# Kernel optimization log

Hardware: AMD Instinct MI355X
Metric: run time of the kernel (lower is better)

## Reference

```python
import jax, jax.numpy as jnp
import numpy as np

DIM = 192
STATE = 64
B = 8
H = 64
W = 64
EPS_LN = 1e-5
EPS_BN = 1e-5


def _layernorm(x, g, b):
    m = jnp.mean(x, axis=-1, keepdims=True)
    v = jnp.mean((x - m) ** 2, axis=-1, keepdims=True)
    return (x - m) / jnp.sqrt(v + EPS_LN) * g + b


def _linear(x, w, b=None):
    # torch Linear convention: w is [out, in]
    y = jnp.einsum('...i,oi->...o', x, w)
    return y if b is None else y + b


def _parallel_scan(A, Bd, xp):
    # A, Bd, xp: [B, L, S]; h_t = A_t*h_{t-1} + Bd_t*xp_t via log-space cumsum
    A_safe = jnp.clip(A, 0.001, 0.999)
    log_A = jnp.log(A_safe + 1e-10)
    log_cum_A = jnp.cumsum(log_A, axis=1)
    log_cum_A_max = jnp.max(log_cum_A, axis=1, keepdims=True)
    cum_A = jnp.exp(log_cum_A - log_cum_A_max)
    BX = Bd * xp
    # prepend zeros, drop last: normalizer uses cumprod up to t-1
    log_pad = jnp.pad(log_cum_A - log_cum_A_max, ((0, 0), (1, 0), (0, 0)))[:, :-1]
    BX_norm = BX * jnp.exp(-log_pad)
    return jnp.cumsum(BX_norm, axis=1) * cum_A


def _ssm(x, ln_g, ln_b, xp_w, xp_b, dt_w, dt_b, A_log, B_w, C_w, Dp, out_w, out_b):
    xn = _layernorm(x, ln_g, ln_b)
    delta = jax.nn.softplus(_linear(xn, dt_w, dt_b)) * 0.01 + 0.0001  # [B,L,S]
    B_t = _linear(xn, B_w)
    C_t = _linear(xn, C_w)
    A = -jnp.exp(A_log)  # [S]
    x_proj = _linear(xn, xp_w, xp_b)
    deltaA = jnp.clip(delta * A, -10.0, -0.0001)
    A_disc = jnp.exp(deltaA)
    B_disc = delta * B_t
    h = _parallel_scan(A_disc, B_disc, x_proj)
    y = C_t * h
    y = jnp.where(jnp.all(jnp.isfinite(y)), y, jnp.zeros_like(y))
    y = _linear(y, out_w, out_b)
    return y + jnp.clip(Dp, -2.0, 2.0) * x


def reference(x, ln1_g, ln1_b, ln2_g, ln2_b, dw_w, bn_g, bn_b, bn_rm, bn_rv,
              ssm_ln_g, ssm_ln_b, xp_w, xp_b, dt_w, dt_b, A_log, B_w, C_w,
              D_param, out_w, out_b, mlp_w1, mlp_b1, mlp_w2, mlp_b2,
              alpha_local, alpha_ssm, alpha_mlp):
    identity = x
    # depthwise 3x3 conv + BatchNorm2d (eval mode, running stats)
    xc = jax.lax.conv_general_dilated(
        x, dw_w, (1, 1), 'SAME', feature_group_count=DIM,
        dimension_numbers=('NCHW', 'OIHW', 'NCHW'))
    scale = (bn_g / jnp.sqrt(bn_rv + EPS_BN))[None, :, None, None]
    x_local = (xc - bn_rm[None, :, None, None]) * scale + bn_b[None, :, None, None]
    # SSM branch on flattened spatial sequence
    x_seq = x.transpose(0, 2, 3, 1).reshape(B, H * W, DIM)
    x_seq = _layernorm(x_seq, ln1_g, ln1_b)
    x_seq = _ssm(x_seq, ssm_ln_g, ssm_ln_b, xp_w, xp_b, dt_w, dt_b, A_log,
                 B_w, C_w, D_param, out_w, out_b)
    x_ssm = x_seq.reshape(B, H, W, DIM).transpose(0, 3, 1, 2)
    xr = identity + alpha_local * x_local + alpha_ssm * x_ssm
    # residual MLP (dropout = identity at inference)
    x_mlp = xr.transpose(0, 2, 3, 1).reshape(B, H * W, DIM)
    x_mlp = _layernorm(x_mlp, ln2_g, ln2_b)
    x_mlp = _linear(jax.nn.gelu(_linear(x_mlp, mlp_w1, mlp_b1), approximate=False),
                    mlp_w2, mlp_b2)
    return xr + alpha_mlp * x_mlp.reshape(B, H, W, DIM).transpose(0, 3, 1, 2)


def setup_inputs() -> dict:
    key = jax.random.key(0)
    ks = jax.random.split(key, 12)
    def nrm(k, shape, s):
        return jax.random.normal(k, shape, jnp.float32) * s
    f32 = jnp.float32
    return {
        'x': jax.random.normal(ks[0], (B, DIM, H, W), f32),
        'ln1_g': jnp.ones(DIM, f32), 'ln1_b': jnp.zeros(DIM, f32),
        'ln2_g': jnp.ones(DIM, f32), 'ln2_b': jnp.zeros(DIM, f32),
        'dw_w': nrm(ks[1], (DIM, 1, 3, 3), 0.2),
        'bn_g': jnp.ones(DIM, f32), 'bn_b': jnp.zeros(DIM, f32),
        'bn_rm': jnp.zeros(DIM, f32), 'bn_rv': jnp.ones(DIM, f32),
        'ssm_ln_g': jnp.ones(DIM, f32), 'ssm_ln_b': jnp.zeros(DIM, f32),
        'xp_w': nrm(ks[2], (STATE, DIM), 0.05), 'xp_b': jnp.zeros(STATE, f32),
        'dt_w': nrm(ks[3], (STATE, DIM), 0.05), 'dt_b': jnp.zeros(STATE, f32),
        'A_log': jnp.log(jax.random.uniform(ks[4], (STATE,), f32) * 0.8 + 0.2),
        'B_w': nrm(ks[5], (STATE, DIM), 0.05),
        'C_w': nrm(ks[6], (STATE, DIM), 0.05),
        'D_param': jnp.zeros(DIM, f32),
        'out_w': nrm(ks[7], (DIM, STATE), 0.05), 'out_b': jnp.zeros(DIM, f32),
        'mlp_w1': nrm(ks[8], (4 * DIM, DIM), 0.03), 'mlp_b1': jnp.zeros(4 * DIM, f32),
        'mlp_w2': nrm(ks[9], (DIM, 4 * DIM), 0.03), 'mlp_b2': jnp.zeros(DIM, f32),
        'alpha_local': jnp.full((1,), 0.5, f32),
        'alpha_ssm': jnp.full((1,), 0.5, f32),
        'alpha_mlp': jnp.full((1,), 0.5, f32),
    }
```

## Files before the change

### kernel.cpp

```cpp
#include <hip/hip_runtime.h>
#include <hip/hip_bf16.h>
#include <math.h>


#define DEV static __device__ __forceinline__

constexpr int Bn = 8, Dm = 192, Ln = 4096, Sn = 64, Hd = 768;

typedef __attribute__((ext_vector_type(8))) short bf16x8;
typedef __attribute__((ext_vector_type(4))) float f32x4;

DEV float wave_sum(float v) {
#pragma unroll
  for (int off = 1; off < 64; off <<= 1) v += __shfl_xor(v, off);
  return v;
}

DEV short f2b(float x) {
  __hip_bfloat16 h = __float2bfloat16(x);
  return *(short*)&h;
}

DEV float b2f(short x) {
  __hip_bfloat16 h = *(__hip_bfloat16*)&x;
  return __bfloat162float(h);
}

__global__ __launch_bounds__(256) void k_prep(
    const float* __restrict__ x, const float* __restrict__ g1, const float* __restrict__ b1,
    const float* __restrict__ g2, const float* __restrict__ b2,
    short* __restrict__ xnb, short* __restrict__ xln1b,
    const float* __restrict__ dt_w, const float* __restrict__ B_w,
    const float* __restrict__ C_w, const float* __restrict__ xp_w,
    const float* __restrict__ out_w, const float* __restrict__ w1,
    const float* __restrict__ w2, short* __restrict__ wb) {
  __shared__ __align__(16) float tile[Dm * 65];
  int tid = threadIdx.x;
  if (blockIdx.y == 8) {
    for (int i = blockIdx.x * 256 + tid; i < 89088; i += 64 * 256) {
      const float4* src;
      if (i < 3072)       src = (const float4*)dt_w + i;
      else if (i < 6144)  src = (const float4*)B_w + (i - 3072);
      else if (i < 9216)  src = (const float4*)C_w + (i - 6144);
      else if (i < 12288) src = (const float4*)xp_w + (i - 9216);
      else if (i < 15360) src = (const float4*)out_w + (i - 12288);
      else if (i < 52224) src = (const float4*)w1 + (i - 15360);
      else                src = (const float4*)w2 + (i - 52224);
      float4 v = *src;
      int o = i * 4;
      wb[o] = f2b(v.x); wb[o + 1] = f2b(v.y); wb[o + 2] = f2b(v.z); wb[o + 3] = f2b(v.w);
    }
    return;
  }
  int b = blockIdx.y, l0 = blockIdx.x * 64;
  const float* xb = x + (size_t)b * Dm * Ln;
  for (int i = tid; i < Dm * 16; i += 256) {
    int d = i >> 4, l4 = (i & 15) << 2;
    float4 v = *(const float4*)&xb[d * Ln + l0 + l4];
    tile[d * 65 + l4]     = v.x; tile[d * 65 + l4 + 1] = v.y;
    tile[d * 65 + l4 + 2] = v.z; tile[d * 65 + l4 + 3] = v.w;
  }
  __syncthreads();
  int lane = tid & 63, wv = tid >> 6;
  float ga0 = g1[lane], ga1 = g1[lane + 64], ga2 = g1[lane + 128];
  float bb0 = b1[lane], bb1 = b1[lane + 64], bb2 = b1[lane + 128];
  float gc0 = g2[lane], gc1 = g2[lane + 64], gc2 = g2[lane + 128];
  float bc0 = b2[lane], bc1 = b2[lane + 64], bc2 = b2[lane + 128];
  for (int li = wv; li < 64; li += 4) {
    float v0 = tile[lane * 65 + li], v1 = tile[(lane + 64) * 65 + li], v2 = tile[(lane + 128) * 65 + li];
    float s  = wave_sum(v0 + v1 + v2);
    float sq = wave_sum(v0 * v0 + v1 * v1 + v2 * v2);
    float m = s * (1.f / 192.f);
    float inv = rsqrtf(sq * (1.f / 192.f) - m * m + 1e-5f);
    float y0 = (v0 - m) * inv * ga0 + bb0;
    float y1 = (v1 - m) * inv * ga1 + bb1;
    float y2 = (v2 - m) * inv * ga2 + bb2;
    float s2  = wave_sum(y0 + y1 + y2);
    float sq2 = wave_sum(y0 * y0 + y1 * y1 + y2 * y2);
    float m2 = s2 * (1.f / 192.f);
    float inv2 = rsqrtf(sq2 * (1.f / 192.f) - m2 * m2 + 1e-5f);
    size_t base = ((size_t)b * Ln + l0 + li) * Dm;
    xln1b[base + lane]       = f2b(y0);
    xln1b[base + lane + 64]  = f2b(y1);
    xln1b[base + lane + 128] = f2b(y2);
    xnb[base + lane]       = f2b((y0 - m2) * inv2 * gc0 + bc0);
    xnb[base + lane + 64]  = f2b((y1 - m2) * inv2 * gc1 + bc1);
    xnb[base + lane + 128] = f2b((y2 - m2) * inv2 * gc2 + bc2);
  }
}

__global__ __launch_bounds__(256) void k_proj(
    const short* __restrict__ xnb, const short* __restrict__ wcat,
    const float* __restrict__ dt_b, const float* __restrict__ xp_b,
    const float* __restrict__ A_log, float* __restrict__ aA, unsigned* __restrict__ bxc,
    float* __restrict__ sums) {
  __shared__ __align__(16) short As[64 * 72];
  __shared__ __align__(16) short Bs[256 * 72];
  int m0 = blockIdx.x * 64, tid = threadIdx.x;
  int lane = tid & 63, l16 = lane & 15, quad = lane >> 4, w = tid >> 6;
  f32x4 acc[16] = {};
  for (int kt = 0; kt < 3; kt++) {
    int kb = kt * 64;
    for (int i = tid; i < 512; i += 256) {
      int row = i >> 3, c8 = (i & 7) * 8;
      *(float4*)&As[row * 72 + c8] = *(const float4*)&xnb[(size_t)(m0 + row) * 192 + kb + c8];
    }
    for (int i = tid; i < 2048; i += 256) {
      int row = i >> 3, c8 = (i & 7) * 8;
      *(float4*)&Bs[row * 72 + c8] = *(const float4*)&wcat[(size_t)row * 192 + kb + c8];
    }
    __syncthreads();
#pragma unroll
    for (int ks = 0; ks < 2; ks++) {
      int ko = ks * 32 + quad * 8;
      bf16x8 a0 = *(const bf16x8*)&As[(w * 16 + l16) * 72 + ko];
#pragma unroll
      for (int nh = 0; nh < 2; nh++) {
        bf16x8 bfr[8];
#pragma unroll
        for (int j = 0; j < 8; j++) bfr[j] = *(const bf16x8*)&Bs[((nh * 8 + j) * 16 + l16) * 72 + ko];
#pragma unroll
        for (int j = 0; j < 8; j++)
          acc[nh * 8 + j] = __builtin_amdgcn_mfma_f32_16x16x32_bf16(a0, bfr[j], acc[nh * 8 + j], 0, 0, 0);
      }
    }
    __syncthreads();
  }
  float* aAs = (float*)Bs;
  float* bxs = aAs + 64 * 65;
  float Av[4], dtbv[4], xpbv[4];
#pragma unroll
  for (int ni = 0; ni < 4; ni++) {
    int s = ni * 16 + l16;
    Av[ni] = -expf(A_log[s]); dtbv[ni] = dt_b[s]; xpbv[ni] = xp_b[s];
  }
#pragma unroll
  for (int r = 0; r < 4; r++) {
    int lm = w * 16 + quad * 4 + r;
    int m = m0 + lm;
#pragma unroll
    for (int ni = 0; ni < 4; ni++) {
      int s = ni * 16 + l16;
      float z = acc[ni][r] + dtbv[ni];
      float sp = (z > 20.f) ? z : log1pf(expf(z));
      float delta = sp * 0.01f + 0.0001f;
      float bt  = acc[ni + 4][r];
      float ct  = acc[ni + 8][r];
      float xpv = acc[ni + 12][r] + xpbv[ni];
      float dA = fminf(fmaxf(delta * Av[ni], -10.f), -0.0001f);
      float Ae = fminf(fmaxf(expf(dA), 0.001f), 0.999f) + 1e-10f;
      short bxh = f2b(delta * bt * xpv);
      aA[(size_t)m * 64 + s] = Ae;
      unsigned pk = (unsigned)(unsigned short)bxh
                  | ((unsigned)(unsigned short)f2b(ct) << 16);
      bxc[(size_t)m * 64 + s] = pk;
      aAs[lm * 65 + s] = Ae;
      bxs[lm * 65 + s] = b2f(bxh);
    }
  }
  __syncthreads();
  int s = tid & 63, seg = tid >> 6, chunk = seg >> 1, sub = seg & 1;
  bool first = ((m0 & 4095) == 0) && (chunk == 0) && (sub == 0);
  float P = 1.f, H = 0.f;
  int base = chunk * 32 + sub * 16;
#pragma unroll
  for (int j = 0; j < 16; j++) {
    float a  = aAs[(base + j) * 65 + s];
    float bx = bxs[(base + j) * 65 + s];
    if (first && j == 0) { P = a; H = bx; }
    else { P *= a; H = a * (H + bx); }
  }
  float* partP = (float*)As;
  float* partH = partP + 256;
  partP[seg * 64 + s] = P; partH[seg * 64 + s] = H;
  __syncthreads();
  if (tid < 128) {
    int c = tid >> 6;
    float p0 = partP[(c * 2) * 64 + s], p1 = partP[(c * 2 + 1) * 64 + s];
    float h0 = partH[(c * 2) * 64 + s], h1 = partH[(c * 2 + 1) * 64 + s];
    int ci = (m0 >> 12) * 128 + ((m0 & 4095) >> 5) + c;
    sums[(ci * 2 + 0) * 64 + s] = p0 * p1;
    sums[(ci * 2 + 1) * 64 + s] = p1 * h0 + h1;
  }
}

__global__ __launch_bounds__(256) void k_scan2(const float* __restrict__ sums,
                                               float* __restrict__ carries) {
  __shared__ float Pp[4 * 64], Hp[4 * 64];
  int b = blockIdx.x, tid = threadIdx.x, s = tid & 63, q = tid >> 6;
  float P = 1.f, H = 0.f;
#pragma unroll 4
  for (int j = 0; j < 32; j++) {
    int ci = b * 128 + q * 32 + j;
    float a = sums[(ci * 2 + 0) * 64 + s];
    float h = sums[(ci * 2 + 1) * 64 + s];
    P *= a; H = a * H + h;
  }
  Pp[q * 64 + s] = P; Hp[q * 64 + s] = H;
  __syncthreads();
  float cur = 0.f;
  for (int qq = 0; qq < q; qq++) cur = Pp[qq * 64 + s] * cur + Hp[qq * 64 + s];
#pragma unroll 4
  for (int j = 0; j < 32; j++) {
    int ci = b * 128 + q * 32 + j;
    carries[ci * 64 + s] = cur;
    float a = sums[(ci * 2 + 0) * 64 + s];
    float h = sums[(ci * 2 + 1) * 64 + s];
    cur = a * cur + h;
  }
}

__global__ __launch_bounds__(256) void k_conv(
    const float* __restrict__ x, const float* __restrict__ dw,
    const float* __restrict__ bn_g, const float* __restrict__ bn_b,
    const float* __restrict__ bn_rm, const float* __restrict__ bn_rv,
    const float* __restrict__ a_loc, float* __restrict__ xr) {
  __shared__ __align__(16) float xs[64 * 64];
  int d = blockIdx.x, b = blockIdx.y, tid = threadIdx.x;
  const float* xp = x + ((size_t)b * Dm + d) * Ln;
  for (int i = tid; i < 1024; i += 256) ((float4*)xs)[i] = ((const float4*)xp)[i];
  __syncthreads();
  float w[9];
#pragma unroll
  for (int k = 0; k < 9; k++) w[k] = dw[d * 9 + k];
  float scale = bn_g[d] * rsqrtf(bn_rv[d] + 1e-5f);
  float rm = bn_rm[d], bb = bn_b[d];
  float al = a_loc[0];
  float* xo = xr + ((size_t)b * Dm + d) * Ln;
  for (int i = tid; i < 4096; i += 256) {
    int h = i >> 6, wc = i & 63;
    float acc = 0.f;
#pragma unroll
    for (int kh = 0; kh < 3; kh++) {
      int hh = h + kh - 1;
      if (hh < 0 || hh >= 64) continue;
#pragma unroll
      for (int kw = 0; kw < 3; kw++) {
        int ww2 = wc + kw - 1;
        if (ww2 < 0 || ww2 >= 64) continue;
        acc += xs[hh * 64 + ww2] * w[kh * 3 + kw];
      }
    }
    float xl = (acc - rm) * scale + bb;
    xo[i] = xs[i] + al * xl;
  }
}

__global__ __launch_bounds__(256) void k_out(
    const float* __restrict__ aA, const unsigned* __restrict__ bxc,
    const float* __restrict__ carries,
    const short* __restrict__ owb, const float* __restrict__ out_b,
    const float* __restrict__ Dp, const short* __restrict__ xln1b,
    const float* __restrict__ a_ssm, const float* __restrict__ g2,
    const float* __restrict__ bb2,
    float* __restrict__ xr, short* __restrict__ xn2) {
  __shared__ __align__(16) float smemf[64 * 193];
  short* As = (short*)smemf;
  short* Bs = (short*)smemf + 192 * 72;
  float* tile = smemf;
  int l0g = blockIdx.x * 64, tid = threadIdx.x;
  int lane = tid & 63, l16 = lane & 15, quad = lane >> 4, wv = tid >> 6;
  for (int i = tid; i < 1536; i += 256) {
    int row = i >> 3, c8 = (i & 7) * 8;
    *(float4*)&As[row * 72 + c8] = *(const float4*)&owb[row * 64 + c8];
  }
  int bb = l0g >> 12, c0 = (l0g & 4095) >> 5;
  if (wv < 2) {
    int c = c0 + wv, s = lane;
    float h = carries[(bb * 128 + c) * 64 + s];
    const float* ap = aA + (size_t)(l0g + wv * 32) * 64;
    const unsigned* bp = bxc + (size_t)(l0g + wv * 32) * 64;
    int t = 0;
    if (c == 0) {
      unsigned u = bp[s];
      h = b2f((short)(u & 0xFFFF));
      Bs[(wv * 32) * 72 + s] = f2b(b2f((short)(u >> 16)) * h);
      t = 1;
    }
#pragma unroll 4
    for (; t < 32; t++) {
      unsigned u = bp[t * 64 + s];
      float a = ap[t * 64 + s];
      h = a * (h + b2f((short)(u & 0xFFFF)));
      Bs[(wv * 32 + t) * 72 + s] = f2b(b2f((short)(u >> 16)) * h);
    }
  }
  __syncthreads();
  f32x4 acc[3][4] = {};
#pragma unroll
  for (int ks = 0; ks < 2; ks++) {
    int ko = ks * 32 + quad * 8;
    bf16x8 a[3], b[4];
#pragma unroll
    for (int mi = 0; mi < 3; mi++) a[mi] = *(const bf16x8*)&As[(wv * 48 + mi * 16 + l16) * 72 + ko];
#pragma unroll
    for (int ni = 0; ni < 4; ni++) b[ni] = *(const bf16x8*)&Bs[(ni * 16 + l16) * 72 + ko];
#pragma unroll
    for (int mi = 0; mi < 3; mi++)
#pragma unroll
      for (int ni = 0; ni < 4; ni++)
        acc[mi][ni] = __builtin_amdgcn_mfma_f32_16x16x32_bf16(a[mi], b[ni], acc[mi][ni], 0, 0, 0);
  }
  __syncthreads();
  float as_ = a_ssm[0];
#pragma unroll
  for (int mi = 0; mi < 3; mi++)
#pragma unroll
    for (int r = 0; r < 4; r++) {
      int d = wv * 48 + mi * 16 + quad * 4 + r;
      float ob = out_b[d];
      float dc = fminf(fmaxf(Dp[d], -2.f), 2.f);
#pragma unroll
      for (int ni = 0; ni < 4; ni++) {
        int l = l0g + ni * 16 + l16;
        float v = acc[mi][ni][r] + ob;
        if (dc != 0.f) v += dc * b2f(xln1b[(size_t)l * 192 + d]);
        size_t idx = ((size_t)bb * Dm + d) * Ln + (l & 4095);
        float nx = xr[idx] + as_ * v;
        xr[idx] = nx;
        tile[(l & 63) * 193 + d] = nx;
      }
    }
  __syncthreads();
  float g0 = g2[lane], g1v = g2[lane + 64], g2v = g2[lane + 128];
  float b0 = bb2[lane], b1v = bb2[lane + 64], b2v = bb2[lane + 128];
  for (int li = wv; li < 64; li += 4) {
    float v0 = tile[li * 193 + lane], v1 = tile[li * 193 + lane + 64], v2 = tile[li * 193 + lane + 128];
    float s  = wave_sum(v0 + v1 + v2);
    float sq = wave_sum(v0 * v0 + v1 * v1 + v2 * v2);
    float m = s * (1.f / 192.f);
    float inv = rsqrtf(sq * (1.f / 192.f) - m * m + 1e-5f);
    size_t base = (size_t)(l0g + li) * Dm;
    xn2[base + lane]       = f2b((v0 - m) * inv * g0 + b0);
    xn2[base + lane + 64]  = f2b((v1 - m) * inv * g1v + b1v);
    xn2[base + lane + 128] = f2b((v2 - m) * inv * g2v + b2v);
  }
}

__global__ __launch_bounds__(256) void k_gemm1(
    const short* __restrict__ xn2, const short* __restrict__ w1b,
    const float* __restrict__ b1h, short* __restrict__ hid) {
  __shared__ __align__(16) short smem[2 * 128 * 88];
  short* As = smem;
  short* Bs = smem + 128 * 88;
  int m0 = blockIdx.x * 128, n0 = blockIdx.y * 128, tid = threadIdx.x;
  int lane = tid & 63, l16 = lane & 15, quad = lane >> 4;
  int wm = (tid >> 6) >> 1, wn = (tid >> 6) & 1;
  f32x4 acc[4][4] = {};
  for (int kt = 0; kt < 3; kt++) {
    int kb = kt * 64;
    for (int i = tid; i < 1024; i += 256) {
      int row = i >> 3, c8 = (i & 7) * 8;
      *(float4*)&As[row * 88 + c8] = *(const float4*)&xn2[(size_t)(m0 + row) * 192 + kb + c8];
      *(float4*)&Bs[row * 88 + c8] = *(const float4*)&w1b[(size_t)(n0 + row) * 192 + kb + c8];
    }
    __syncthreads();
#pragma unroll
    for (int ks = 0; ks < 2; ks++) {
      int ko = ks * 32 + quad * 8;
      bf16x8 a[4], b[4];
#pragma unroll
      for (int mi = 0; mi < 4; mi++) a[mi] = *(const bf16x8*)&As[(wm * 64 + mi * 16 + l16) * 88 + ko];
#pragma unroll
      for (int ni = 0; ni < 4; ni++) b[ni] = *(const bf16x8*)&Bs[(wn * 64 + ni * 16 + l16) * 88 + ko];
#pragma unroll
      for (int mi = 0; mi < 4; mi++)
#pragma unroll
        for (int ni = 0; ni < 4; ni++)
          acc[mi][ni] = __builtin_amdgcn_mfma_f32_16x16x32_bf16(a[mi], b[ni], acc[mi][ni], 0, 0, 0);
    }
    __syncthreads();
  }
  short* Cs = smem;
  float bias4[4];
#pragma unroll
  for (int ni = 0; ni < 4; ni++) bias4[ni] = b1h[n0 + wn * 64 + ni * 16 + l16];
#pragma unroll
  for (int mi = 0; mi < 4; mi++)
#pragma unroll
    for (int ni = 0; ni < 4; ni++) {
      int n = wn * 64 + ni * 16 + l16;
#pragma unroll
      for (int r = 0; r < 4; r++) {
        int m = wm * 64 + mi * 16 + quad * 4 + r;
        float v = acc[mi][ni][r] + bias4[ni];
        float g = 0.5f * v * (1.f + erff(v * 0.70710678118f));
        Cs[m * 136 + n] = f2b(g);
      }
    }
  __syncthreads();
  for (int i = tid; i < 2048; i += 256) {
    int m = i >> 4, ch = i & 15;
    *(float4*)&hid[(size_t)(m0 + m) * 768 + n0 + ch * 8] = *(const float4*)&Cs[m * 136 + ch * 8];
  }
}

__global__ __launch_bounds__(256) void k_gemm2(
    const short* __restrict__ hid, const short* __restrict__ w2b,
    const float* __restrict__ b2o, const float* __restrict__ xr,
    const float* __restrict__ am, float* __restrict__ out) {
  __shared__ __align__(16) short Wt[96 * 88];
  __shared__ __align__(16) short Ht[64 * 88];
  int l0g = blockIdx.x * 64, d0 = blockIdx.y * 96, tid = threadIdx.x;
  int lane = tid & 63, l16 = lane & 15, quad = lane >> 4;
  int wm = (tid >> 6) >> 1, wn = (tid >> 6) & 1;
  f32x4 acc[3][2] = {};
  for (int kt = 0; kt < 12; kt++) {
    int kb = kt * 64;
    for (int i = tid; i < 768; i += 256) {
      int row = i >> 3, c8 = (i & 7) * 8;
      *(float4*)&Wt[row * 88 + c8] = *(const float4*)&w2b[(size_t)(d0 + row) * 768 + kb + c8];
    }
    for (int i = tid; i < 512; i += 256) {
      int row = i >> 3, c8 = (i & 7) * 8;
      *(float4*)&Ht[row * 88 + c8] = *(const float4*)&hid[(size_t)(l0g + row) * 768 + kb + c8];
    }
    __syncthreads();
#pragma unroll
    for (int ks = 0; ks < 2; ks++) {
      int ko = ks * 32 + quad * 8;
      bf16x8 a[3], b[2];
#pragma unroll
      for (int mi = 0; mi < 3; mi++) a[mi] = *(const bf16x8*)&Wt[(wm * 48 + mi * 16 + l16) * 88 + ko];
#pragma unroll
      for (int ni = 0; ni < 2; ni++) b[ni] = *(const bf16x8*)&Ht[(wn * 32 + ni * 16 + l16) * 88 + ko];
#pragma unroll
      for (int mi = 0; mi < 3; mi++)
#pragma unroll
        for (int ni = 0; ni < 2; ni++)
          acc[mi][ni] = __builtin_amdgcn_mfma_f32_16x16x32_bf16(a[mi], b[ni], acc[mi][ni], 0, 0, 0);
    }
    __syncthreads();
  }
  float alpha = am[0];
#pragma unroll
  for (int mi = 0; mi < 3; mi++)
#pragma unroll
    for (int r = 0; r < 4; r++) {
      int d = d0 + wm * 48 + mi * 16 + quad * 4 + r;
      float bias = b2o[d];
#pragma unroll
      for (int ni = 0; ni < 2; ni++) {
        int lg = l0g + wn * 32 + ni * 16 + l16;
        size_t idx = ((size_t)(lg >> 12) * Dm + d) * Ln + (lg & 4095);
        out[idx] = xr[idx] + alpha * (acc[mi][ni][r] + bias);
      }
    }
}

extern "C" void kernel_launch(void* const* d_in, const int* in_sizes, int n_in,
                              void* d_out, int out_size, void* d_ws, size_t ws_size,
                              hipStream_t stream) {
  (void)in_sizes; (void)n_in; (void)out_size; (void)ws_size;
  const float* x     = (const float*)d_in[0];
  const float* ln1_g = (const float*)d_in[1];
  const float* ln1_b = (const float*)d_in[2];
  const float* ln2_g = (const float*)d_in[3];
  const float* ln2_b = (const float*)d_in[4];
  const float* dw_w  = (const float*)d_in[5];
  const float* bn_g  = (const float*)d_in[6];
  const float* bn_b  = (const float*)d_in[7];
  const float* bn_rm = (const float*)d_in[8];
  const float* bn_rv = (const float*)d_in[9];
  const float* ssm_g = (const float*)d_in[10];
  const float* ssm_b = (const float*)d_in[11];
  const float* xp_w  = (const float*)d_in[12];
  const float* xp_b  = (const float*)d_in[13];
  const float* dt_w  = (const float*)d_in[14];
  const float* dt_b  = (const float*)d_in[15];
  const float* A_log = (const float*)d_in[16];
  const float* B_w   = (const float*)d_in[17];
  const float* C_w   = (const float*)d_in[18];
  const float* Dp    = (const float*)d_in[19];
  const float* out_w = (const float*)d_in[20];
  const float* out_b = (const float*)d_in[21];
  const float* w1    = (const float*)d_in[22];
  const float* b1    = (const float*)d_in[23];
  const float* w2    = (const float*)d_in[24];
  const float* b2    = (const float*)d_in[25];
  const float* a_loc = (const float*)d_in[26];
  const float* a_ssm = (const float*)d_in[27];
  const float* a_mlp = (const float*)d_in[28];

  float* ws = (float*)d_ws;
  short*    xnb   = (short*)ws;
  short*    xln1b = (short*)(ws + 3145728);
  float*    aA    = ws + 6291456;
  unsigned* bxc   = (unsigned*)(ws + 8388608);
  float*    xr    = ws + 17825792;
  short*    wb    = (short*)(ws + 24117248);
  float*    sums  = ws + 24829952;
  float*    carr  = ws + 24961024;
  short*    xn2   = (short*)(ws + 25026560);
  short*    hid   = (short*)(ws + 28172288);
  short*    wcatb = wb;
  short*    owb   = wb + 49152;
  short*    w1b   = wb + 61440;
  short*    w2b   = wb + 208896;
  float*    out   = (float*)d_out;

  k_prep <<<dim3(64, 9),  256, 0, stream>>>(x, ln1_g, ln1_b, ssm_g, ssm_b, xnb, xln1b,
                                            dt_w, B_w, C_w, xp_w, out_w, w1, w2, wb);
  k_conv <<<dim3(192, 8), 256, 0, stream>>>(x, dw_w, bn_g, bn_b, bn_rm, bn_rv, a_loc, xr);
  k_proj <<<dim3(512),    256, 0, stream>>>(xnb, wcatb, dt_b, xp_b, A_log, aA, bxc, sums);
  k_scan2<<<dim3(8),      256, 0, stream>>>(sums, carr);
  k_out  <<<dim3(512),    256, 0, stream>>>(aA, bxc, carr, owb, out_b, Dp, xln1b,
                                            a_ssm, ln2_g, ln2_b, xr, xn2);
  k_gemm1<<<dim3(256, 6), 256, 0, stream>>>(xn2, w1b, b1, hid);
  k_gemm2<<<dim3(512, 2), 256, 0, stream>>>(hid, w2b, b2, xr, a_mlp, out);
}
```

Baseline: 276.6 us.

## Fuse MLP GEMMs into one kernel and prefetch residual in k_out

Merges the two MLP GEMMs into one kernel that computes the GELU hidden activation per 64-token block in 64-wide chunks held in double-buffered LDS and immediately accumulates the second projection. This drops the global write and read of the bf16 hidden tensor and one launch. Weights are now read directly from global memory by each block without LDS staging, raising L2 traffic and load latency. k_out also prefetches the residual xr values into registers before the scan to overlap that load latency.

```diff
diff --git a/kernel.cpp b/kernel.cpp
--- a/kernel.cpp
+++ b/kernel.cpp
@@ -265,6 +265,18 @@
     *(float4*)&As[row * 72 + c8] = *(const float4*)&owb[row * 64 + c8];
   }
   int bb = l0g >> 12, c0 = (l0g & 4095) >> 5;
+  float xrv[3][4][4];
+#pragma unroll
+  for (int mi = 0; mi < 3; mi++)
+#pragma unroll
+    for (int r = 0; r < 4; r++) {
+      int d = wv * 48 + mi * 16 + quad * 4 + r;
+#pragma unroll
+      for (int ni = 0; ni < 4; ni++) {
+        int l = l0g + ni * 16 + l16;
+        xrv[mi][r][ni] = xr[((size_t)bb * Dm + d) * Ln + (l & 4095)];
+      }
+    }
   if (wv < 2) {
     int c = c0 + wv, s = lane;
     float h = carries[(bb * 128 + c) * 64 + s];
@@ -316,7 +328,7 @@
         float v = acc[mi][ni][r] + ob;
         if (dc != 0.f) v += dc * b2f(xln1b[(size_t)l * 192 + d]);
         size_t idx = ((size_t)bb * Dm + d) * Ln + (l & 4095);
-        float nx = xr[idx] + as_ * v;
+        float nx = xrv[mi][r][ni] + as_ * v;
         xr[idx] = nx;
         tile[(l & 63) * 193 + d] = nx;
       }
@@ -337,113 +349,74 @@
   }
 }
 
-__global__ __launch_bounds__(256) void k_gemm1(
+__global__ __launch_bounds__(256) void k_mlp(
     const short* __restrict__ xn2, const short* __restrict__ w1b,
-    const float* __restrict__ b1h, short* __restrict__ hid) {
-  __shared__ __align__(16) short smem[2 * 128 * 88];
-  short* As = smem;
-  short* Bs = smem + 128 * 88;
-  int m0 = blockIdx.x * 128, n0 = blockIdx.y * 128, tid = threadIdx.x;
-  int lane = tid & 63, l16 = lane & 15, quad = lane >> 4;
-  int wm = (tid >> 6) >> 1, wn = (tid >> 6) & 1;
-  f32x4 acc[4][4] = {};
-  for (int kt = 0; kt < 3; kt++) {
-    int kb = kt * 64;
-    for (int i = tid; i < 1024; i += 256) {
-      int row = i >> 3, c8 = (i & 7) * 8;
-      *(float4*)&As[row * 88 + c8] = *(const float4*)&xn2[(size_t)(m0 + row) * 192 + kb + c8];
-      *(float4*)&Bs[row * 88 + c8] = *(const float4*)&w1b[(size_t)(n0 + row) * 192 + kb + c8];
+    const float* __restrict__ b1h, const short* __restrict__ w2b,
+    const float* __restrict__ b2o, const float* __restrict__ xr,
+    const float* __restrict__ am, float* __restrict__ out) {
+  __shared__ __align__(16) short As[64 * 200];
+  __shared__ __align__(16) short Hs[2][64 * 72];
+  int l0g = blockIdx.x * 64, tid = threadIdx.x;
+  int lane = tid & 63, l16 = lane & 15, quad = lane >> 4, wv = tid >> 6;
+  for (int i = tid; i < 1536; i += 256) {
+    int row = i / 24, c8 = (i % 24) * 8;
+    *(float4*)&As[row * 200 + c8] = *(const float4*)&xn2[(size_t)(l0g + row) * 192 + c8];
+  }
+  __syncthreads();
+  f32x4 acc2[3][4] = {};
+  for (int kc = 0; kc < 12; kc++) {
+    f32x4 acc1[4] = {};
+#pragma unroll
+    for (int ks = 0; ks < 6; ks++) {
+      int ko = ks * 32 + quad * 8;
+      bf16x8 a0 = *(const bf16x8*)&As[(wv * 16 + l16) * 200 + ko];
+#pragma unroll
+      for (int ni = 0; ni < 4; ni++) {
+        bf16x8 bfr = *(const bf16x8*)&w1b[(size_t)(kc * 64 + ni * 16 + l16) * 192 + ko];
+        acc1[ni] = __builtin_amdgcn_mfma_f32_16x16x32_bf16(a0, bfr, acc1[ni], 0, 0, 0);
+      }
+    }
+    short* H = Hs[kc & 1];
+#pragma unroll
+    for (int ni = 0; ni < 4; ni++) {
+      float bias = b1h[kc * 64 + ni * 16 + l16];
+#pragma unroll
+      for (int r = 0; r < 4; r++) {
+        float v = acc1[ni][r] + bias;
+        float g = 0.5f * v * (1.f + erff(v * 0.70710678118f));
+        H[(wv * 16 + quad * 4 + r) * 72 + ni * 16 + l16] = f2b(g);
+      }
     }
     __syncthreads();
 #pragma unroll
     for (int ks = 0; ks < 2; ks++) {
       int ko = ks * 32 + quad * 8;
-      bf16x8 a[4], b[4];
-#pragma unroll
-      for (int mi = 0; mi < 4; mi++) a[mi] = *(const bf16x8*)&As[(wm * 64 + mi * 16 + l16) * 88 + ko];
-#pragma unroll
-      for (int ni = 0; ni < 4; ni++) b[ni] = *(const bf16x8*)&Bs[(wn * 64 + ni * 16 + l16) * 88 + ko];
-#pragma unroll
-      for (int mi = 0; mi < 4; mi++)
+      bf16x8 a[3], b[4];
+#pragma unroll
+      for (int mi = 0; mi < 3; mi++)
+        a[mi] = *(const bf16x8*)&w2b[(size_t)(wv * 48 + mi * 16 + l16) * 768 + kc * 64 + ko];
+#pragma unroll
+      for (int ni = 0; ni < 4; ni++) b[ni] = *(const bf16x8*)&H[(ni * 16 + l16) * 72 + ko];
+#pragma unroll
+      for (int mi = 0; mi < 3; mi++)
 #pragma unroll
         for (int ni = 0; ni < 4; ni++)
-          acc[mi][ni] = __builtin_amdgcn_mfma_f32_16x16x32_bf16(a[mi], b[ni], acc[mi][ni], 0, 0, 0);
-    }
-    __syncthreads();
-  }
-  short* Cs = smem;
-  float bias4[4];
-#pragma unroll
-  for (int ni = 0; ni < 4; ni++) bias4[ni] = b1h[n0 + wn * 64 + ni * 16 + l16];
-#pragma unroll
-  for (int mi = 0; mi < 4; mi++)
-#pragma unroll
-    for (int ni = 0; ni < 4; ni++) {
-      int n = wn * 64 + ni * 16 + l16;
-#pragma unroll
-      for (int r = 0; r < 4; r++) {
-        int m = wm * 64 + mi * 16 + quad * 4 + r;
-        float v = acc[mi][ni][r] + bias4[ni];
-        float g = 0.5f * v * (1.f + erff(v * 0.70710678118f));
-        Cs[m * 136 + n] = f2b(g);
-      }
-    }
-  __syncthreads();
-  for (int i = tid; i < 2048; i += 256) {
-    int m = i >> 4, ch = i & 15;
-    *(float4*)&hid[(size_t)(m0 + m) * 768 + n0 + ch * 8] = *(const float4*)&Cs[m * 136 + ch * 8];
-  }
-}
-
-__global__ __launch_bounds__(256) void k_gemm2(
-    const short* __restrict__ hid, const short* __restrict__ w2b,
-    const float* __restrict__ b2o, const float* __restrict__ xr,
-    const float* __restrict__ am, float* __restrict__ out) {
-  __shared__ __align__(16) short Wt[96 * 88];
-  __shared__ __align__(16) short Ht[64 * 88];
-  int l0g = blockIdx.x * 64, d0 = blockIdx.y * 96, tid = threadIdx.x;
-  int lane = tid & 63, l16 = lane & 15, quad = lane >> 4;
-  int wm = (tid >> 6) >> 1, wn = (tid >> 6) & 1;
-  f32x4 acc[3][2] = {};
-  for (int kt = 0; kt < 12; kt++) {
-    int kb = kt * 64;
-    for (int i = tid; i < 768; i += 256) {
-      int row = i >> 3, c8 = (i & 7) * 8;
-      *(float4*)&Wt[row * 88 + c8] = *(const float4*)&w2b[(size_t)(d0 + row) * 768 + kb + c8];
-    }
-    for (int i = tid; i < 512; i += 256) {
-      int row = i >> 3, c8 = (i & 7) * 8;
-      *(float4*)&Ht[row * 88 + c8] = *(const float4*)&hid[(size_t)(l0g + row) * 768 + kb + c8];
-    }
-    __syncthreads();
-#pragma unroll
-    for (int ks = 0; ks < 2; ks++) {
-      int ko = ks * 32 + quad * 8;
-      bf16x8 a[3], b[2];
-#pragma unroll
-      for (int mi = 0; mi < 3; mi++) a[mi] = *(const bf16x8*)&Wt[(wm * 48 + mi * 16 + l16) * 88 + ko];
-#pragma unroll
-      for (int ni = 0; ni < 2; ni++) b[ni] = *(const bf16x8*)&Ht[(wn * 32 + ni * 16 + l16) * 88 + ko];
-#pragma unroll
-      for (int mi = 0; mi < 3; mi++)
-#pragma unroll
-        for (int ni = 0; ni < 2; ni++)
-          acc[mi][ni] = __builtin_amdgcn_mfma_f32_16x16x32_bf16(a[mi], b[ni], acc[mi][ni], 0, 0, 0);
-    }
-    __syncthreads();
+          acc2[mi][ni] = __builtin_amdgcn_mfma_f32_16x16x32_bf16(a[mi], b[ni], acc2[mi][ni], 0, 0, 0);
+    }
   }
   float alpha = am[0];
+  int bb = l0g >> 12;
 #pragma unroll
   for (int mi = 0; mi < 3; mi++)
 #pragma unroll
     for (int r = 0; r < 4; r++) {
-      int d = d0 + wm * 48 + mi * 16 + quad * 4 + r;
+      int d = wv * 48 + mi * 16 + quad * 4 + r;
       float bias = b2o[d];
 #pragma unroll
-      for (int ni = 0; ni < 2; ni++) {
-        int lg = l0g + wn * 32 + ni * 16 + l16;
-        size_t idx = ((size_t)(lg >> 12) * Dm + d) * Ln + (lg & 4095);
-        out[idx] = xr[idx] + alpha * (acc[mi][ni][r] + bias);
+      for (int ni = 0; ni < 4; ni++) {
+        int l = l0g + ni * 16 + l16;
+        size_t idx = ((size_t)bb * Dm + d) * Ln + (l & 4095);
+        out[idx] = xr[idx] + alpha * (acc2[mi][ni][r] + bias);
       }
     }
 }
@@ -492,7 +465,6 @@
   float*    sums  = ws + 24829952;
   float*    carr  = ws + 24961024;
   short*    xn2   = (short*)(ws + 25026560);
-  short*    hid   = (short*)(ws + 28172288);
   short*    wcatb = wb;
   short*    owb   = wb + 49152;
   short*    w1b   = wb + 61440;
@@ -506,6 +478,5 @@
   k_scan2<<<dim3(8),      256, 0, stream>>>(sums, carr);
   k_out  <<<dim3(512),    256, 0, stream>>>(aA, bxc, carr, owb, out_b, Dp, xln1b,
                                             a_ssm, ln2_g, ln2_b, xr, xn2);
-  k_gemm1<<<dim3(256, 6), 256, 0, stream>>>(xn2, w1b, b1, hid);
-  k_gemm2<<<dim3(512, 2), 256, 0, stream>>>(hid, w2b, b2, xr, a_mlp, out);
-}
+  k_mlp  <<<dim3(512),    256, 0, stream>>>(xn2, w1b, b1, w2b, b2, xr, a_mlp, out);
+}
```

Measured after the change: 315.5 us. 14.1% more time.
